# Kernel tuning notes

Measured on AMD Instinct MI355X. Metric: run time of the kernel, lower is better.

## Reference

```python
import jax, jax.numpy as jnp
import numpy as np

N_NODES = 100000
N_EDGES = 3200000
EMB = 256
OUT = 256


def setup_inputs() -> dict:
    key = jax.random.key(0)
    k1, k2, k3, k4, k5 = jax.random.split(key, 5)
    embeddings = jax.random.normal(k1, (N_NODES, EMB), dtype=jnp.float32)
    adj_rows = jax.random.randint(k2, (N_EDGES,), 0, N_NODES, dtype=jnp.int32)
    adj_cols = jax.random.randint(k3, (N_EDGES,), 0, N_NODES, dtype=jnp.int32)
    adj_vals = jax.random.uniform(k4, (N_EDGES,), dtype=jnp.float32)
    W = jax.random.normal(k5, (EMB, OUT), dtype=jnp.float32) * 0.02
    return {
        "embeddings": embeddings,
        "adj_rows": adj_rows,
        "adj_cols": adj_cols,
        "adj_vals": adj_vals,
        "W": W,
    }


def reference(embeddings, adj_rows, adj_cols, adj_vals, W):
    # SpMM: agg[i] = sum_{e: rows[e]==i} vals[e] * embeddings[cols[e]]
    messages = adj_vals[:, None] * embeddings[adj_cols]  # [E, EMB]
    agg = jax.ops.segment_sum(messages, adj_rows, num_segments=embeddings.shape[0])  # [N, EMB]
    # Dense projection + ReLU
    out = jax.nn.relu(agg @ W)  # [N, OUT]
    return out
```

## Files before the change

kernel.cpp:

```cpp
#include <hip/hip_runtime.h>
#include <stdint.h>


typedef unsigned short u16;
typedef __attribute__((ext_vector_type(8))) short short8v;
typedef __attribute__((ext_vector_type(4))) float f32x4;

#define RBSH 8
#define RB 256
#define NBMAX 512
#define MS_T 2048
#define MS_PT 8

__device__ __forceinline__ float b2f(u16 u) {
  union { unsigned i; float f; } x; x.i = ((unsigned)u) << 16; return x.f;
}
__device__ __forceinline__ u16 f2b(float f) {
  union { unsigned i; float f; } x; x.f = f;
  unsigned r = x.i + 0x7fffu + ((x.i >> 16) & 1u);
  return (u16)(r >> 16);
}
__device__ __forceinline__ float blo(unsigned u) {
  union { unsigned i; float f; } x; x.i = u << 16; return x.f;
}
__device__ __forceinline__ float bhi(unsigned u) {
  union { unsigned i; float f; } x; x.i = u & 0xFFFF0000u; return x.f;
}

__global__ __launch_bounds__(256) void count_k(const int* __restrict__ rows,
                                               const unsigned* __restrict__ valsw,
                                               int* __restrict__ flag,
                                               int* __restrict__ cnt, int E, int NB) {
  __shared__ int h[NBMAX];
  __shared__ int dcnt;
  int tid = threadIdx.x;
  for (int b = tid; b < NB; b += 256) h[b] = 0;
  if (blockIdx.x == 0 && tid == 0) dcnt = 0;
  __syncthreads();
  if (blockIdx.x == 0) {
    int dlim = E < 4096 ? E : 4096;
    int c = 0;
    for (int i = tid; i < dlim; i += 256) {
      unsigned w = valsw[i];
      if ((w & 0xFFFFu) >= 0x3F80u) c++;
    }
    atomicAdd(&dcnt, c);
  }
  int base = blockIdx.x * MS_T;
#pragma unroll
  for (int i = 0; i < MS_PT; ++i) {
    int e = base + i * 256 + tid;
    if (e < E) atomicAdd(&h[rows[e] >> RBSH], 1);
  }
  __syncthreads();
  for (int b = tid; b < NB; b += 256) cnt[(size_t)blockIdx.x * NB + b] = h[b];
  if (blockIdx.x == 0 && tid == 0) {
    int dlim = E < 4096 ? E : 4096;
    *flag = (dcnt < (dlim >> 2)) ? 1 : 0;
  }
}

__global__ __launch_bounds__(256) void rowscan_k(int* __restrict__ cnt,
                                                 int* __restrict__ totals,
                                                 int NB, int NBLK) {
  __shared__ int part[256];
  int b = blockIdx.x, tid = threadIdx.x;
  int K = (NBLK + 255) >> 8;
  int lo = tid * K;
  int v[8];
  int s = 0;
#pragma unroll
  for (int u = 0; u < 8; ++u) {
    int i = lo + u;
    v[u] = (u < K && i < NBLK) ? cnt[(size_t)i * NB + b] : 0;
    s += v[u];
  }
  part[tid] = s;
  __syncthreads();
  for (int o = 1; o < 256; o <<= 1) {
    int t = (tid >= o) ? part[tid - o] : 0;
    __syncthreads();
    part[tid] += t;
    __syncthreads();
  }
  int run = part[tid] - s;
#pragma unroll
  for (int u = 0; u < 8; ++u) {
    int i = lo + u;
    if (u < K && i < NBLK) cnt[(size_t)i * NB + b] = run;
    run += v[u];
  }
  if (tid == 255) totals[b] = part[255];
}

__global__ __launch_bounds__(512) void boffscan_k(const int* __restrict__ totals,
                                                  int* __restrict__ boffs, int NB) {
  __shared__ int part[512];
  int tid = threadIdx.x;
  int c = (tid < NB) ? totals[tid] : 0;
  part[tid] = c;
  __syncthreads();
  for (int o = 1; o < 512; o <<= 1) {
    int t = (tid >= o) ? part[tid - o] : 0;
    __syncthreads();
    part[tid] += t;
    __syncthreads();
  }
  if (tid < NB) boffs[tid] = part[tid] - c;
  if (tid == 511) boffs[NB] = part[511];
}

__global__ __launch_bounds__(256) void place_k(const int* __restrict__ flag,
                                               const int* __restrict__ rows,
                                               const int* __restrict__ cols,
                                               const void* __restrict__ valsv,
                                               const int* __restrict__ base,
                                               const int* __restrict__ boffs,
                                               int2* __restrict__ pack, int E, int NB) {
  __shared__ int hist[NBMAX + 1];
  __shared__ int gbase[NBMAX];
  __shared__ int part[256];
  __shared__ int2 buf[MS_T];
  __shared__ u16 brow[MS_T];
  int isbf = *flag;
  int tid = threadIdx.x;
  int tbase = blockIdx.x * MS_T;

  for (int b = tid; b <= NB; b += 256) hist[b] = 0;
  for (int b = tid; b < NB; b += 256)
    gbase[b] = boffs[b] + base[(size_t)blockIdx.x * NB + b];
  __syncthreads();

  int bk[MS_PT], ofs[MS_PT], cl[MS_PT], vb[MS_PT];
#pragma unroll
  for (int i = 0; i < MS_PT; ++i) {
    int e = tbase + i * 256 + tid;
    if (e < E) {
      int r = rows[e];
      bk[i] = r >> RBSH;
      cl[i] = cols[e] | ((r & (RB - 1)) << 17);
      float v;
      if (isbf) v = b2f(((const u16*)valsv)[e]);
      else      v = ((const float*)valsv)[e];
      vb[i] = __float_as_int(v);
      ofs[i] = atomicAdd(&hist[bk[i]], 1);
    } else {
      bk[i] = -1; ofs[i] = 0; cl[i] = 0; vb[i] = 0;
    }
  }
  __syncthreads();

  int K = (NB + 255) >> 8;
  int lo = tid * K, hi = lo + K;
  if (hi > NB) hi = NB;
  if (lo > NB) lo = NB;
  int s = 0;
  for (int b = lo; b < hi; ++b) s += hist[b];
  part[tid] = s;
  __syncthreads();
  for (int o = 1; o < 256; o <<= 1) {
    int v = (tid >= o) ? part[tid - o] : 0;
    __syncthreads();
    part[tid] += v;
    __syncthreads();
  }
  int run = part[tid] - s;
  for (int b = lo; b < hi; ++b) {
    int c = hist[b];
    hist[b] = run;
    run += c;
  }
  if (tid == 255) hist[NB] = part[255];
  __syncthreads();

#pragma unroll
  for (int i = 0; i < MS_PT; ++i) {
    if (bk[i] >= 0) {
      int slot = hist[bk[i]] + ofs[i];
      buf[slot] = make_int2(cl[i], vb[i]);
      brow[slot] = (u16)bk[i];
    }
  }
  __syncthreads();

  int tot = hist[NB];
  for (int i = tid; i < tot; i += 256) {
    int b = brow[i];
    pack[gbase[b] + (i - hist[b])] = buf[i];
  }
}

__global__ __launch_bounds__(512) void ms2_k(const int* __restrict__ boffs,
                                             const int2* __restrict__ pack,
                                             int2* __restrict__ pack2,
                                             int* __restrict__ offs, int N, int NB) {
  __shared__ int bins[RB];
  __shared__ int part[256];
  int b = blockIdx.x;
  int tid = threadIdx.x;
  int beg = boffs[b], end = boffs[b + 1];
  if (tid < RB) bins[tid] = 0;
  __syncthreads();
  for (int i = beg + tid; i < end; i += 512)
    atomicAdd(&bins[(pack[i].x >> 17) & (RB - 1)], 1);
  __syncthreads();
  int c = (tid < 256) ? bins[tid] : 0;
  if (tid < 256) part[tid] = c;
  __syncthreads();
  for (int o = 1; o < 256; o <<= 1) {
    int v = (tid < 256 && tid >= o) ? part[tid - o] : 0;
    __syncthreads();
    if (tid < 256) part[tid] += v;
    __syncthreads();
  }
  if (tid < 256) {
    int pfx = part[tid] - c;
    int n = b * RB + tid;
    if (n < N) offs[n] = beg + pfx;
    bins[tid] = pfx;
  }
  if (b == NB - 1 && tid == 0) offs[N] = end;
  __syncthreads();
  for (int i = beg + tid; i < end; i += 512) {
    int2 q = pack[i];
    int r = (q.x >> 17) & (RB - 1);
    int p = atomicAdd(&bins[r], 1);
    pack2[beg + p] = q;
  }
}

__global__ void wtr_k(const int* __restrict__ flag, const void* __restrict__ Wv,
                      u16* __restrict__ Wt) {
  int isbf = *flag;
  int i = blockIdx.x * 256 + threadIdx.x;
  int n = i >> 8, k = i & 255;
  float w;
  if (isbf) w = b2f(((const u16*)Wv)[k * 256 + n]);
  else      w = ((const float*)Wv)[k * 256 + n];
  Wt[n * 256 + k] = f2b(w);
}

__global__ __launch_bounds__(256) void proj_k(const int* __restrict__ flag,
                                              const void* __restrict__ embv,
                                              const u16* __restrict__ Wt,
                                              u16* __restrict__ P, int N) {
  int isbf = *flag;
  int wave = threadIdx.x >> 6, lane = threadIdx.x & 63;
  int lr = lane & 15, lq = lane >> 4;
  int m0 = blockIdx.x * 64;
  int n0 = wave * 64;

  f32x4 acc[4][4];
#pragma unroll
  for (int mi = 0; mi < 4; ++mi)
#pragma unroll
    for (int ni = 0; ni < 4; ++ni) acc[mi][ni] = (f32x4)0.f;

  int arow[4];
#pragma unroll
  for (int mi = 0; mi < 4; ++mi) {
    int r = m0 + mi * 16 + lr;
    arow[mi] = r < N ? r : N - 1;
  }

  for (int ks = 0; ks < 8; ++ks) {
    int kb = ks * 32 + lq * 8;
    short8v a[4], b[4];
#pragma unroll
    for (int mi = 0; mi < 4; ++mi) {
      if (isbf) {
        a[mi] = *(const short8v*)((const u16*)embv + (size_t)arow[mi] * 256 + kb);
      } else {
        const float* p = (const float*)embv + (size_t)arow[mi] * 256 + kb;
        float4 x = *(const float4*)p;
        float4 y = *(const float4*)(p + 4);
        short8v t;
        t[0] = (short)f2b(x.x); t[1] = (short)f2b(x.y);
        t[2] = (short)f2b(x.z); t[3] = (short)f2b(x.w);
        t[4] = (short)f2b(y.x); t[5] = (short)f2b(y.y);
        t[6] = (short)f2b(y.z); t[7] = (short)f2b(y.w);
        a[mi] = t;
      }
    }
#pragma unroll
    for (int ni = 0; ni < 4; ++ni)
      b[ni] = *(const short8v*)(Wt + (size_t)(n0 + ni * 16 + lr) * 256 + kb);
#pragma unroll
    for (int mi = 0; mi < 4; ++mi)
#pragma unroll
      for (int ni = 0; ni < 4; ++ni)
        acc[mi][ni] = __builtin_amdgcn_mfma_f32_16x16x32_bf16(a[mi], b[ni], acc[mi][ni], 0, 0, 0);
  }

#pragma unroll
  for (int mi = 0; mi < 4; ++mi) {
    int rbase = m0 + mi * 16 + lq * 4;
#pragma unroll
    for (int ni = 0; ni < 4; ++ni) {
      int col = n0 + ni * 16 + lr;
#pragma unroll
      for (int r = 0; r < 4; ++r) {
        int row = rbase + r;
        if (row < N) P[(size_t)row * 256 + col] = f2b(acc[mi][ni][r]);
      }
    }
  }
}

__global__ __launch_bounds__(256) void agg_k(const int* __restrict__ flag,
                                             const u16* __restrict__ P,
                                             const int* __restrict__ offs,
                                             const int2* __restrict__ pack,
                                             void* __restrict__ outv, int N) {
  int outbf = *flag;
  int wave = threadIdx.x >> 6, lane = threadIdx.x & 63;
  int node = blockIdx.x * 4 + wave;
  if (node >= N) return;
  int sub = lane & 31, half = lane >> 5;
  int beg = offs[node], end = offs[node + 1];
  const u16* pb = P + sub * 8;

  float acc[8];
#pragma unroll
  for (int k = 0; k < 8; ++k) acc[k] = 0.f;

  for (int j = beg; j < end; j += 16) {
#define LDQ(k) int i##k = j + 2 * k + half; \
               int2 q##k = pack[i##k < end ? i##k : end - 1];
    LDQ(0) LDQ(1) LDQ(2) LDQ(3) LDQ(4) LDQ(5) LDQ(6) LDQ(7)
#undef LDQ
    __builtin_amdgcn_sched_barrier(0);
#define LDU(k) int4 u##k = *(const int4*)(pb + (size_t)(q##k.x & 0x1FFFF) * 256); \
               float v##k = i##k < end ? __int_as_float(q##k.y) : 0.f;
    LDU(0) LDU(1) LDU(2) LDU(3) LDU(4) LDU(5) LDU(6) LDU(7)
#undef LDU
    __builtin_amdgcn_sched_barrier(0);
#define FMA8(k) { unsigned ux = (unsigned)u##k.x, uy = (unsigned)u##k.y; \
                  unsigned uz = (unsigned)u##k.z, uw = (unsigned)u##k.w; \
                  acc[0] += v##k * blo(ux); acc[1] += v##k * bhi(ux); \
                  acc[2] += v##k * blo(uy); acc[3] += v##k * bhi(uy); \
                  acc[4] += v##k * blo(uz); acc[5] += v##k * bhi(uz); \
                  acc[6] += v##k * blo(uw); acc[7] += v##k * bhi(uw); }
    FMA8(0) FMA8(1) FMA8(2) FMA8(3) FMA8(4) FMA8(5) FMA8(6) FMA8(7)
#undef FMA8
  }

#pragma unroll
  for (int k = 0; k < 8; ++k) acc[k] += __shfl(acc[k], lane ^ 32);

#pragma unroll
  for (int k = 0; k < 8; ++k) acc[k] = fmaxf(acc[k], 0.f);
  int d0 = sub * 8 + half * 4;
  if (outbf) {
    ushort4 o;
    o.x = f2b(acc[half * 4 + 0]); o.y = f2b(acc[half * 4 + 1]);
    o.z = f2b(acc[half * 4 + 2]); o.w = f2b(acc[half * 4 + 3]);
    *(ushort4*)((u16*)outv + (size_t)node * 256 + d0) = o;
  } else {
    float4 o;
    o.x = acc[half * 4 + 0]; o.y = acc[half * 4 + 1];
    o.z = acc[half * 4 + 2]; o.w = acc[half * 4 + 3];
    *(float4*)((float*)outv + (size_t)node * 256 + d0) = o;
  }
}


extern "C" void kernel_launch(void* const* d_in, const int* in_sizes, int n_in,
                              void* d_out, int out_size, void* d_ws, size_t ws_size,
                              hipStream_t stream) {
  const void* emb  = d_in[0];
  const int*  rows = (const int*)d_in[1];
  const int*  cols = (const int*)d_in[2];
  const void* vals = d_in[3];
  const void* W    = d_in[4];

  int N = in_sizes[0] / 256;
  int E = in_sizes[1];
  int NB = (N + RB - 1) >> RBSH;
  int NBLK = (E + MS_T - 1) / MS_T;

  char* ws = (char*)d_ws;
  size_t off = 0;
  auto carve = [&](size_t bytes) -> char* {
    char* p = ws + off;
    off += (bytes + 511) & ~(size_t)511;
    return p;
  };
  int*  flag   = (int*) carve(4);
  int*  cnt    = (int*) carve((size_t)NBLK * NB * 4);
  int*  totals = (int*) carve((size_t)NB * 4);
  int*  boffs  = (int*) carve((size_t)(NB + 1) * 4);
  int*  offs   = (int*) carve((size_t)(N + 1) * 4);
  int2* pack   = (int2*)carve((size_t)E * 8);
  int2* pack2  = (int2*)carve((size_t)E * 8);
  u16*  P      = (u16*) carve((size_t)N * 256 * 2);
  u16*  Wt     = (u16*) carve((size_t)256 * 256 * 2);
  (void)ws_size; (void)n_in; (void)out_size;

  count_k<<<NBLK, 256, 0, stream>>>(rows, (const unsigned*)vals, flag, cnt, E, NB);
  rowscan_k<<<NB, 256, 0, stream>>>(cnt, totals, NB, NBLK);
  boffscan_k<<<1, 512, 0, stream>>>(totals, boffs, NB);

  wtr_k<<<256, 256, 0, stream>>>(flag, W, Wt);

  int pb = (N + 63) / 64;
  proj_k<<<pb, 256, 0, stream>>>(flag, emb, Wt, P, N);

  place_k<<<NBLK, 256, 0, stream>>>(flag, rows, cols, vals, cnt, boffs, pack, E, NB);

  ms2_k<<<NB, 512, 0, stream>>>(boffs, pack, pack2, offs, N, NB);

  int ab = (N + 3) / 4;
  agg_k<<<ab, 256, 0, stream>>>(flag, P, offs, pack2, d_out, N);
}
```

Baseline: 566.9 us.

## Fuse W transpose into count kernel, inline bucket scan, retile projection and aggregation

The weight transpose is folded into the counting kernel as extra blocks that recompute the dtype flag locally. The single-block bucket-offset scan kernel is removed; place_k and ms2_k each redo the small prefix scan over bucket totals. Together these drop two kernel launches at the cost of redundant per-block scan work. The projection kernel is retiled so each wave covers 16 rows by all 256 columns, and the aggregation loop processes 32 edges per iteration with byte-offset addressing and a launch-bounds occupancy hint, which raises register pressure.

```diff
diff --git a/kernel.cpp b/kernel.cpp
--- a/kernel.cpp
+++ b/kernel.cpp
@@ -27,13 +27,35 @@
   union { unsigned i; float f; } x; x.i = u & 0xFFFF0000u; return x.f;
 }
 
-__global__ __launch_bounds__(256) void count_k(const int* __restrict__ rows,
-                                               const unsigned* __restrict__ valsw,
-                                               int* __restrict__ flag,
-                                               int* __restrict__ cnt, int E, int NB) {
+__global__ __launch_bounds__(256) void cw_k(const int* __restrict__ rows,
+                                            const unsigned* __restrict__ valsw,
+                                            const void* __restrict__ Wv,
+                                            int* __restrict__ flag,
+                                            int* __restrict__ cnt,
+                                            u16* __restrict__ Wt,
+                                            int E, int NB, int NBLK) {
   __shared__ int h[NBMAX];
   __shared__ int dcnt;
   int tid = threadIdx.x;
+  if (blockIdx.x >= NBLK) {
+    if (tid == 0) dcnt = 0;
+    __syncthreads();
+    int dlim = E < 4096 ? E : 4096;
+    int c = 0;
+    for (int i = tid; i < dlim; i += 256) {
+      unsigned w = valsw[i];
+      if ((w & 0xFFFFu) >= 0x3F80u) c++;
+    }
+    atomicAdd(&dcnt, c);
+    __syncthreads();
+    int isbf = (dcnt < (dlim >> 2)) ? 1 : 0;
+    int w = blockIdx.x - NBLK;
+    float x;
+    if (isbf) x = b2f(((const u16*)Wv)[tid * 256 + w]);
+    else      x = ((const float*)Wv)[tid * 256 + w];
+    Wt[w * 256 + tid] = f2b(x);
+    return;
+  }
   for (int b = tid; b < NB; b += 256) h[b] = 0;
   if (blockIdx.x == 0 && tid == 0) dcnt = 0;
   __syncthreads();
@@ -93,21 +115,53 @@
   if (tid == 255) totals[b] = part[255];
 }
 
-__global__ __launch_bounds__(512) void boffscan_k(const int* __restrict__ totals,
-                                                  int* __restrict__ boffs, int NB) {
-  __shared__ int part[512];
-  int tid = threadIdx.x;
-  int c = (tid < NB) ? totals[tid] : 0;
-  part[tid] = c;
-  __syncthreads();
-  for (int o = 1; o < 512; o <<= 1) {
-    int t = (tid >= o) ? part[tid - o] : 0;
-    __syncthreads();
-    part[tid] += t;
-    __syncthreads();
-  }
-  if (tid < NB) boffs[tid] = part[tid] - c;
-  if (tid == 511) boffs[NB] = part[511];
+__global__ __launch_bounds__(256) void proj_k(const int* __restrict__ flag,
+                                              const void* __restrict__ embv,
+                                              const u16* __restrict__ Wt,
+                                              u16* __restrict__ P, int N) {
+  int isbf = *flag;
+  int wave = threadIdx.x >> 6, lane = threadIdx.x & 63;
+  int lr = lane & 15, lq = lane >> 4;
+  int m0 = blockIdx.x * 64 + wave * 16;
+  int arow = m0 + lr;
+  if (arow >= N) arow = N - 1;
+
+  f32x4 acc[16];
+#pragma unroll
+  for (int ni = 0; ni < 16; ++ni) acc[ni] = (f32x4)0.f;
+
+  for (int ks = 0; ks < 8; ++ks) {
+    int kb = ks * 32 + lq * 8;
+    short8v a;
+    if (isbf) {
+      a = *(const short8v*)((const u16*)embv + (size_t)arow * 256 + kb);
+    } else {
+      const float* p = (const float*)embv + (size_t)arow * 256 + kb;
+      float4 x = *(const float4*)p;
+      float4 y = *(const float4*)(p + 4);
+      short8v t;
+      t[0] = (short)f2b(x.x); t[1] = (short)f2b(x.y);
+      t[2] = (short)f2b(x.z); t[3] = (short)f2b(x.w);
+      t[4] = (short)f2b(y.x); t[5] = (short)f2b(y.y);
+      t[6] = (short)f2b(y.z); t[7] = (short)f2b(y.w);
+      a = t;
+    }
+#pragma unroll
+    for (int ni = 0; ni < 16; ++ni) {
+      short8v b = *(const short8v*)(Wt + (size_t)(ni * 16 + lr) * 256 + kb);
+      acc[ni] = __builtin_amdgcn_mfma_f32_16x16x32_bf16(a, b, acc[ni], 0, 0, 0);
+    }
+  }
+
+#pragma unroll
+  for (int ni = 0; ni < 16; ++ni) {
+    int col = ni * 16 + lr;
+#pragma unroll
+    for (int r = 0; r < 4; ++r) {
+      int row = m0 + lq * 4 + r;
+      if (row < N) P[(size_t)row * 256 + col] = f2b(acc[ni][r]);
+    }
+  }
 }
 
 __global__ __launch_bounds__(256) void place_k(const int* __restrict__ flag,
@@ -115,7 +169,7 @@
                                                const int* __restrict__ cols,
                                                const void* __restrict__ valsv,
                                                const int* __restrict__ base,
-                                               const int* __restrict__ boffs,
+                                               const int* __restrict__ totals,
                                                int2* __restrict__ pack, int E, int NB) {
   __shared__ int hist[NBMAX + 1];
   __shared__ int gbase[NBMAX];
@@ -126,9 +180,37 @@
   int tid = threadIdx.x;
   int tbase = blockIdx.x * MS_T;
 
+  {
+    int K2 = (NB + 255) >> 8;
+    int t0 = tid * K2;
+    int tv[2];
+    int ss = 0;
+#pragma unroll
+    for (int u = 0; u < 2; ++u) {
+      int i = t0 + u;
+      tv[u] = (u < K2 && i < NB) ? totals[i] : 0;
+      ss += tv[u];
+    }
+    part[tid] = ss;
+    __syncthreads();
+    for (int o = 1; o < 256; o <<= 1) {
+      int v = (tid >= o) ? part[tid - o] : 0;
+      __syncthreads();
+      part[tid] += v;
+      __syncthreads();
+    }
+    int run = part[tid] - ss;
+#pragma unroll
+    for (int u = 0; u < 2; ++u) {
+      int i = t0 + u;
+      if (u < K2 && i < NB) gbase[i] = run;
+      run += tv[u];
+    }
+  }
+  __syncthreads();
+  for (int b = tid; b < NB; b += 256)
+    gbase[b] += base[(size_t)blockIdx.x * NB + b];
   for (int b = tid; b <= NB; b += 256) hist[b] = 0;
-  for (int b = tid; b < NB; b += 256)
-    gbase[b] = boffs[b] + base[(size_t)blockIdx.x * NB + b];
   __syncthreads();
 
   int bk[MS_PT], ofs[MS_PT], cl[MS_PT], vb[MS_PT];
@@ -190,15 +272,28 @@
   }
 }
 
-__global__ __launch_bounds__(512) void ms2_k(const int* __restrict__ boffs,
+__global__ __launch_bounds__(512) void ms2_k(const int* __restrict__ totals,
                                              const int2* __restrict__ pack,
                                              int2* __restrict__ pack2,
                                              int* __restrict__ offs, int N, int NB) {
   __shared__ int bins[RB];
-  __shared__ int part[256];
+  __shared__ int part[512];
   int b = blockIdx.x;
   int tid = threadIdx.x;
-  int beg = boffs[b], end = boffs[b + 1];
+
+  int c0 = (tid < NB) ? totals[tid] : 0;
+  part[tid] = c0;
+  __syncthreads();
+  for (int o = 1; o < 512; o <<= 1) {
+    int v = (tid >= o) ? part[tid - o] : 0;
+    __syncthreads();
+    part[tid] += v;
+    __syncthreads();
+  }
+  int end = part[b];
+  int beg = end - totals[b];
+  __syncthreads();
+
   if (tid < RB) bins[tid] = 0;
   __syncthreads();
   for (int i = beg + tid; i < end; i += 512)
@@ -229,120 +324,49 @@
   }
 }
 
-__global__ void wtr_k(const int* __restrict__ flag, const void* __restrict__ Wv,
-                      u16* __restrict__ Wt) {
-  int isbf = *flag;
-  int i = blockIdx.x * 256 + threadIdx.x;
-  int n = i >> 8, k = i & 255;
-  float w;
-  if (isbf) w = b2f(((const u16*)Wv)[k * 256 + n]);
-  else      w = ((const float*)Wv)[k * 256 + n];
-  Wt[n * 256 + k] = f2b(w);
-}
-
-__global__ __launch_bounds__(256) void proj_k(const int* __restrict__ flag,
-                                              const void* __restrict__ embv,
-                                              const u16* __restrict__ Wt,
-                                              u16* __restrict__ P, int N) {
-  int isbf = *flag;
-  int wave = threadIdx.x >> 6, lane = threadIdx.x & 63;
-  int lr = lane & 15, lq = lane >> 4;
-  int m0 = blockIdx.x * 64;
-  int n0 = wave * 64;
-
-  f32x4 acc[4][4];
-#pragma unroll
-  for (int mi = 0; mi < 4; ++mi)
-#pragma unroll
-    for (int ni = 0; ni < 4; ++ni) acc[mi][ni] = (f32x4)0.f;
-
-  int arow[4];
-#pragma unroll
-  for (int mi = 0; mi < 4; ++mi) {
-    int r = m0 + mi * 16 + lr;
-    arow[mi] = r < N ? r : N - 1;
-  }
-
-  for (int ks = 0; ks < 8; ++ks) {
-    int kb = ks * 32 + lq * 8;
-    short8v a[4], b[4];
-#pragma unroll
-    for (int mi = 0; mi < 4; ++mi) {
-      if (isbf) {
-        a[mi] = *(const short8v*)((const u16*)embv + (size_t)arow[mi] * 256 + kb);
-      } else {
-        const float* p = (const float*)embv + (size_t)arow[mi] * 256 + kb;
-        float4 x = *(const float4*)p;
-        float4 y = *(const float4*)(p + 4);
-        short8v t;
-        t[0] = (short)f2b(x.x); t[1] = (short)f2b(x.y);
-        t[2] = (short)f2b(x.z); t[3] = (short)f2b(x.w);
-        t[4] = (short)f2b(y.x); t[5] = (short)f2b(y.y);
-        t[6] = (short)f2b(y.z); t[7] = (short)f2b(y.w);
-        a[mi] = t;
-      }
-    }
-#pragma unroll
-    for (int ni = 0; ni < 4; ++ni)
-      b[ni] = *(const short8v*)(Wt + (size_t)(n0 + ni * 16 + lr) * 256 + kb);
-#pragma unroll
-    for (int mi = 0; mi < 4; ++mi)
-#pragma unroll
-      for (int ni = 0; ni < 4; ++ni)
-        acc[mi][ni] = __builtin_amdgcn_mfma_f32_16x16x32_bf16(a[mi], b[ni], acc[mi][ni], 0, 0, 0);
-  }
-
-#pragma unroll
-  for (int mi = 0; mi < 4; ++mi) {
-    int rbase = m0 + mi * 16 + lq * 4;
-#pragma unroll
-    for (int ni = 0; ni < 4; ++ni) {
-      int col = n0 + ni * 16 + lr;
-#pragma unroll
-      for (int r = 0; r < 4; ++r) {
-        int row = rbase + r;
-        if (row < N) P[(size_t)row * 256 + col] = f2b(acc[mi][ni][r]);
-      }
-    }
-  }
-}
-
-__global__ __launch_bounds__(256) void agg_k(const int* __restrict__ flag,
-                                             const u16* __restrict__ P,
-                                             const int* __restrict__ offs,
-                                             const int2* __restrict__ pack,
-                                             void* __restrict__ outv, int N) {
+__global__ __launch_bounds__(256, 3) void agg_k(const int* __restrict__ flag,
+                                                const u16* __restrict__ P,
+                                                const int* __restrict__ offs,
+                                                const int2* __restrict__ pack,
+                                                void* __restrict__ outv, int N) {
   int outbf = *flag;
   int wave = threadIdx.x >> 6, lane = threadIdx.x & 63;
   int node = blockIdx.x * 4 + wave;
   if (node >= N) return;
   int sub = lane & 31, half = lane >> 5;
   int beg = offs[node], end = offs[node + 1];
-  const u16* pb = P + sub * 8;
+  const char* Pc = (const char*)P;
+  unsigned slo = (unsigned)(sub << 4);
 
   float acc[8];
 #pragma unroll
   for (int k = 0; k < 8; ++k) acc[k] = 0.f;
 
-  for (int j = beg; j < end; j += 16) {
-#define LDQ(k) int i##k = j + 2 * k + half; \
-               int2 q##k = pack[i##k < end ? i##k : end - 1];
-    LDQ(0) LDQ(1) LDQ(2) LDQ(3) LDQ(4) LDQ(5) LDQ(6) LDQ(7)
-#undef LDQ
+  for (int j = beg; j < end; j += 32) {
+    unsigned voff[16];
+    float v[16];
+#pragma unroll
+    for (int k = 0; k < 16; ++k) {
+      int i = j + 2 * k + half;
+      int2 q = pack[i < end ? i : end - 1];
+      voff[k] = (((unsigned)q.x & 0x1FFFFu) << 9) | slo;
+      v[k] = i < end ? __int_as_float(q.y) : 0.f;
+    }
     __builtin_amdgcn_sched_barrier(0);
-#define LDU(k) int4 u##k = *(const int4*)(pb + (size_t)(q##k.x & 0x1FFFF) * 256); \
-               float v##k = i##k < end ? __int_as_float(q##k.y) : 0.f;
-    LDU(0) LDU(1) LDU(2) LDU(3) LDU(4) LDU(5) LDU(6) LDU(7)
-#undef LDU
+    int4 u[16];
+#pragma unroll
+    for (int k = 0; k < 16; ++k) u[k] = *(const int4*)(Pc + voff[k]);
     __builtin_amdgcn_sched_barrier(0);
-#define FMA8(k) { unsigned ux = (unsigned)u##k.x, uy = (unsigned)u##k.y; \
-                  unsigned uz = (unsigned)u##k.z, uw = (unsigned)u##k.w; \
-                  acc[0] += v##k * blo(ux); acc[1] += v##k * bhi(ux); \
-                  acc[2] += v##k * blo(uy); acc[3] += v##k * bhi(uy); \
-                  acc[4] += v##k * blo(uz); acc[5] += v##k * bhi(uz); \
-                  acc[6] += v##k * blo(uw); acc[7] += v##k * bhi(uw); }
-    FMA8(0) FMA8(1) FMA8(2) FMA8(3) FMA8(4) FMA8(5) FMA8(6) FMA8(7)
-#undef FMA8
+#pragma unroll
+    for (int k = 0; k < 16; ++k) {
+      unsigned ux = (unsigned)u[k].x, uy = (unsigned)u[k].y;
+      unsigned uz = (unsigned)u[k].z, uw = (unsigned)u[k].w;
+      float vk = v[k];
+      acc[0] += vk * blo(ux); acc[1] += vk * bhi(ux);
+      acc[2] += vk * blo(uy); acc[3] += vk * bhi(uy);
+      acc[4] += vk * blo(uz); acc[5] += vk * bhi(uz);
+      acc[6] += vk * blo(uw); acc[7] += vk * bhi(uw);
+    }
   }
 
 #pragma unroll
@@ -389,7 +413,6 @@
   int*  flag   = (int*) carve(4);
   int*  cnt    = (int*) carve((size_t)NBLK * NB * 4);
   int*  totals = (int*) carve((size_t)NB * 4);
-  int*  boffs  = (int*) carve((size_t)(NB + 1) * 4);
   int*  offs   = (int*) carve((size_t)(N + 1) * 4);
   int2* pack   = (int2*)carve((size_t)E * 8);
   int2* pack2  = (int2*)carve((size_t)E * 8);
@@ -397,18 +420,16 @@
   u16*  Wt     = (u16*) carve((size_t)256 * 256 * 2);
   (void)ws_size; (void)n_in; (void)out_size;
 
-  count_k<<<NBLK, 256, 0, stream>>>(rows, (const unsigned*)vals, flag, cnt, E, NB);
+  cw_k<<<NBLK + 256, 256, 0, stream>>>(rows, (const unsigned*)vals, W, flag, cnt,
+                                       Wt, E, NB, NBLK);
   rowscan_k<<<NB, 256, 0, stream>>>(cnt, totals, NB, NBLK);
-  boffscan_k<<<1, 512, 0, stream>>>(totals, boffs, NB);
-
-  wtr_k<<<256, 256, 0, stream>>>(flag, W, Wt);
 
   int pb = (N + 63) / 64;
   proj_k<<<pb, 256, 0, stream>>>(flag, emb, Wt, P, N);
 
-  place_k<<<NBLK, 256, 0, stream>>>(flag, rows, cols, vals, cnt, boffs, pack, E, NB);
-
-  ms2_k<<<NB, 512, 0, stream>>>(boffs, pack, pack2, offs, N, NB);
+  place_k<<<NBLK, 256, 0, stream>>>(flag, rows, cols, vals, cnt, totals, pack, E, NB);
+
+  ms2_k<<<NB, 512, 0, stream>>>(totals, pack, pack2, offs, N, NB);
 
   int ab = (N + 3) / 4;
   agg_k<<<ab, 256, 0, stream>>>(flag, P, offs, pack2, d_out, N);
```

New measurement: 603.4 us. +6.4%, slower.

## Stage projection A tile in LDS, use nontemporal loads/stores and packed FMA

Applied to the files above, without the earlier changes.

Several independent changes. The projection kernel now loads each block's 64-row embedding tile once into shared memory, converting to bf16 there, instead of each wave re-reading and re-converting the same rows from global memory. The streaming reads of the packed edge array and the final output writes use nontemporal hints to reduce cache pollution. The aggregation accumulators become float2 vectors so the compiler can emit packed FMA instructions. The trade-off is extra LDS use, which may lower occupancy in the projection kernel.

```diff
diff --git a/kernel.cpp b/kernel.cpp
--- a/kernel.cpp
+++ b/kernel.cpp
@@ -5,6 +5,7 @@
 typedef unsigned short u16;
 typedef __attribute__((ext_vector_type(8))) short short8v;
 typedef __attribute__((ext_vector_type(4))) float f32x4;
+typedef __attribute__((ext_vector_type(2))) float f32x2;
 
 #define RBSH 8
 #define RB 256
@@ -201,8 +202,10 @@
   int beg = boffs[b], end = boffs[b + 1];
   if (tid < RB) bins[tid] = 0;
   __syncthreads();
-  for (int i = beg + tid; i < end; i += 512)
-    atomicAdd(&bins[(pack[i].x >> 17) & (RB - 1)], 1);
+  for (int i = beg + tid; i < end; i += 512) {
+    long long qq = __builtin_nontemporal_load((const long long*)&pack[i]);
+    atomicAdd(&bins[((int)(unsigned)(qq & 0xFFFFFFFFu) >> 17) & (RB - 1)], 1);
+  }
   __syncthreads();
   int c = (tid < 256) ? bins[tid] : 0;
   if (tid < 256) part[tid] = c;
@@ -240,48 +243,59 @@
   Wt[n * 256 + k] = f2b(w);
 }
 
+#define ALD 264
 __global__ __launch_bounds__(256) void proj_k(const int* __restrict__ flag,
                                               const void* __restrict__ embv,
                                               const u16* __restrict__ Wt,
                                               u16* __restrict__ P, int N) {
+  __shared__ u16 Als[64 * ALD];
   int isbf = *flag;
-  int wave = threadIdx.x >> 6, lane = threadIdx.x & 63;
+  int tid = threadIdx.x;
+  int wave = tid >> 6, lane = tid & 63;
   int lr = lane & 15, lq = lane >> 4;
   int m0 = blockIdx.x * 64;
+
+  {
+    int sr = tid >> 2, sc0 = (tid & 3) * 64;
+    int grow = m0 + sr;
+    if (grow >= N) grow = N - 1;
+    if (isbf) {
+      const u16* src = (const u16*)embv + (size_t)grow * 256 + sc0;
+#pragma unroll
+      for (int c = 0; c < 64; c += 8) {
+        short8v v = __builtin_nontemporal_load((const short8v*)(src + c));
+        *(short8v*)&Als[sr * ALD + sc0 + c] = v;
+      }
+    } else {
+      const float* src = (const float*)embv + (size_t)grow * 256 + sc0;
+#pragma unroll
+      for (int c = 0; c < 64; c += 8) {
+        f32x4 x = __builtin_nontemporal_load((const f32x4*)(src + c));
+        f32x4 y = __builtin_nontemporal_load((const f32x4*)(src + c + 4));
+        short8v t;
+        t[0] = (short)f2b(x[0]); t[1] = (short)f2b(x[1]);
+        t[2] = (short)f2b(x[2]); t[3] = (short)f2b(x[3]);
+        t[4] = (short)f2b(y[0]); t[5] = (short)f2b(y[1]);
+        t[6] = (short)f2b(y[2]); t[7] = (short)f2b(y[3]);
+        *(short8v*)&Als[sr * ALD + sc0 + c] = t;
+      }
+    }
+  }
+  __syncthreads();
+
   int n0 = wave * 64;
-
   f32x4 acc[4][4];
 #pragma unroll
   for (int mi = 0; mi < 4; ++mi)
 #pragma unroll
     for (int ni = 0; ni < 4; ++ni) acc[mi][ni] = (f32x4)0.f;
-
-  int arow[4];
-#pragma unroll
-  for (int mi = 0; mi < 4; ++mi) {
-    int r = m0 + mi * 16 + lr;
-    arow[mi] = r < N ? r : N - 1;
-  }
 
   for (int ks = 0; ks < 8; ++ks) {
     int kb = ks * 32 + lq * 8;
     short8v a[4], b[4];
 #pragma unroll
-    for (int mi = 0; mi < 4; ++mi) {
-      if (isbf) {
-        a[mi] = *(const short8v*)((const u16*)embv + (size_t)arow[mi] * 256 + kb);
-      } else {
-        const float* p = (const float*)embv + (size_t)arow[mi] * 256 + kb;
-        float4 x = *(const float4*)p;
-        float4 y = *(const float4*)(p + 4);
-        short8v t;
-        t[0] = (short)f2b(x.x); t[1] = (short)f2b(x.y);
-        t[2] = (short)f2b(x.z); t[3] = (short)f2b(x.w);
-        t[4] = (short)f2b(y.x); t[5] = (short)f2b(y.y);
-        t[6] = (short)f2b(y.z); t[7] = (short)f2b(y.w);
-        a[mi] = t;
-      }
-    }
+    for (int mi = 0; mi < 4; ++mi)
+      a[mi] = *(const short8v*)&Als[(mi * 16 + lr) * ALD + kb];
 #pragma unroll
     for (int ni = 0; ni < 4; ++ni)
       b[ni] = *(const short8v*)(Wt + (size_t)(n0 + ni * 16 + lr) * 256 + kb);
@@ -320,30 +334,38 @@
   int beg = offs[node], end = offs[node + 1];
   const u16* pb = P + sub * 8;
 
-  float acc[8];
-#pragma unroll
-  for (int k = 0; k < 8; ++k) acc[k] = 0.f;
+  f32x2 acc2[4];
+#pragma unroll
+  for (int k = 0; k < 4; ++k) acc2[k] = (f32x2)0.f;
 
   for (int j = beg; j < end; j += 16) {
 #define LDQ(k) int i##k = j + 2 * k + half; \
-               int2 q##k = pack[i##k < end ? i##k : end - 1];
+               long long w##k = __builtin_nontemporal_load( \
+                   (const long long*)&pack[i##k < end ? i##k : end - 1]);
     LDQ(0) LDQ(1) LDQ(2) LDQ(3) LDQ(4) LDQ(5) LDQ(6) LDQ(7)
 #undef LDQ
     __builtin_amdgcn_sched_barrier(0);
-#define LDU(k) int4 u##k = *(const int4*)(pb + (size_t)(q##k.x & 0x1FFFF) * 256); \
-               float v##k = i##k < end ? __int_as_float(q##k.y) : 0.f;
+#define LDU(k) int4 u##k = *(const int4*)(pb + \
+                   (size_t)((unsigned)(w##k & 0xFFFFFFFFu) & 0x1FFFFu) * 256); \
+               float v##k = i##k < end ? __int_as_float((int)(w##k >> 32)) : 0.f;
     LDU(0) LDU(1) LDU(2) LDU(3) LDU(4) LDU(5) LDU(6) LDU(7)
 #undef LDU
     __builtin_amdgcn_sched_barrier(0);
-#define FMA8(k) { unsigned ux = (unsigned)u##k.x, uy = (unsigned)u##k.y; \
-                  unsigned uz = (unsigned)u##k.z, uw = (unsigned)u##k.w; \
-                  acc[0] += v##k * blo(ux); acc[1] += v##k * bhi(ux); \
-                  acc[2] += v##k * blo(uy); acc[3] += v##k * bhi(uy); \
-                  acc[4] += v##k * blo(uz); acc[5] += v##k * bhi(uz); \
-                  acc[6] += v##k * blo(uw); acc[7] += v##k * bhi(uw); }
+#define FMA8(k) { f32x2 vv; vv[0] = v##k; vv[1] = v##k; \
+                  f32x2 p0, p1, p2, p3; \
+                  p0[0] = blo((unsigned)u##k.x); p0[1] = bhi((unsigned)u##k.x); \
+                  p1[0] = blo((unsigned)u##k.y); p1[1] = bhi((unsigned)u##k.y); \
+                  p2[0] = blo((unsigned)u##k.z); p2[1] = bhi((unsigned)u##k.z); \
+                  p3[0] = blo((unsigned)u##k.w); p3[1] = bhi((unsigned)u##k.w); \
+                  acc2[0] += vv * p0; acc2[1] += vv * p1; \
+                  acc2[2] += vv * p2; acc2[3] += vv * p3; }
     FMA8(0) FMA8(1) FMA8(2) FMA8(3) FMA8(4) FMA8(5) FMA8(6) FMA8(7)
 #undef FMA8
   }
+
+  float acc[8];
+#pragma unroll
+  for (int k = 0; k < 8; ++k) acc[k] = acc2[k >> 1][k & 1];
 
 #pragma unroll
   for (int k = 0; k < 8; ++k) acc[k] += __shfl(acc[k], lane ^ 32);
@@ -352,15 +374,15 @@
   for (int k = 0; k < 8; ++k) acc[k] = fmaxf(acc[k], 0.f);
   int d0 = sub * 8 + half * 4;
   if (outbf) {
-    ushort4 o;
-    o.x = f2b(acc[half * 4 + 0]); o.y = f2b(acc[half * 4 + 1]);
-    o.z = f2b(acc[half * 4 + 2]); o.w = f2b(acc[half * 4 + 3]);
-    *(ushort4*)((u16*)outv + (size_t)node * 256 + d0) = o;
+    union { ushort4 o; long long ll; } u;
+    u.o.x = f2b(acc[half * 4 + 0]); u.o.y = f2b(acc[half * 4 + 1]);
+    u.o.z = f2b(acc[half * 4 + 2]); u.o.w = f2b(acc[half * 4 + 3]);
+    __builtin_nontemporal_store(u.ll, (long long*)((u16*)outv + (size_t)node * 256 + d0));
   } else {
-    float4 o;
-    o.x = acc[half * 4 + 0]; o.y = acc[half * 4 + 1];
-    o.z = acc[half * 4 + 2]; o.w = acc[half * 4 + 3];
-    *(float4*)((float*)outv + (size_t)node * 256 + d0) = o;
+    f32x4 o;
+    o[0] = acc[half * 4 + 0]; o[1] = acc[half * 4 + 1];
+    o[2] = acc[half * 4 + 2]; o[3] = acc[half * 4 + 3];
+    __builtin_nontemporal_store(o, (f32x4*)((float*)outv + (size_t)node * 256 + d0));
   }
 }
 
```

After: 583.8 us. 1.03x slower.
